# Kernel optimization log

Measured on AMD Instinct MI355X. Metric: run time of the kernel, lower is better.

The kernel has to match this reference:

```python
import math
import jax, jax.numpy as jnp
import numpy as np

EMBED = 1024
HEAD = 1024  # embedding_dim // num_heads with num_heads=1


def setup_inputs() -> dict:
    key = jax.random.key(0)
    kx, kq, kk, kv = jax.random.split(key, 4)
    x = jax.random.normal(kx, (8, 2048, EMBED), dtype=jnp.float32)
    padding_mask = jnp.ones((8, 2048), dtype=jnp.float32)
    Q = 0.02 * jax.random.normal(kq, (EMBED, HEAD), dtype=jnp.float32)
    K = 0.02 * jax.random.normal(kk, (EMBED, HEAD), dtype=jnp.float32)
    V = 0.02 * jax.random.normal(kv, (EMBED, HEAD), dtype=jnp.float32)
    return {"x": x, "padding_mask": padding_mask, "Q": Q, "K": K, "V": V}


def reference(x, padding_mask, Q, K, V):
    # x: [B, S, E]; Q/K/V: [E, H]; padding_mask: [B, S]
    q = x @ Q  # [B, S, H]
    k = x @ K
    v = x @ V
    scores = jnp.einsum("bsh,bth->bst", q, k)  # [B, S, S]
    # faithful to torch: mask = tril(scores) * padding_mask.unsqueeze(1)
    mask = jnp.tril(scores) * padding_mask[:, None, :]
    scores = jnp.where(mask == 0, -1e9, scores)
    weights = jax.nn.softmax(scores / math.sqrt(k.shape[-1]), axis=-1)
    return weights @ v  # [B, S, H]
```

## Files before the change

kernel.cpp:

```cpp
#include <hip/hip_runtime.h>
#include <hip/hip_bf16.h>


using bf16 = __hip_bfloat16;
typedef __attribute__((ext_vector_type(8))) short short8;
typedef __attribute__((ext_vector_type(4))) unsigned short ushort4_t;
typedef __attribute__((ext_vector_type(4))) float f32x4;

#define BATCH 8
#define SEQ   2048
#define EMB   1024
#define HEADD 1024

__device__ __forceinline__ unsigned short f2bf(float x) {
  bf16 h = __float2bfloat16(x);
  return *reinterpret_cast<unsigned short*>(&h);
}
__device__ __forceinline__ float bf2f(unsigned short u) {
  unsigned int v = ((unsigned int)u) << 16;
  return *reinterpret_cast<float*>(&v);
}

__device__ __forceinline__ void gload_lds16(const bf16* g, bf16* l) {
  __builtin_amdgcn_global_load_lds(
      (const __attribute__((address_space(1))) void*)g,
      (__attribute__((address_space(3))) void*)l, 16, 0, 0);
}

__device__ __forceinline__ int xcd_swz(int wg, int nwg) {
  int q = nwg >> 3, r = nwg & 7;
  int x = wg & 7, o = wg >> 3;
  return (x < r ? x * (q + 1) : r * (q + 1) + (x - r) * q) + o;
}

__global__ __launch_bounds__(256) void cast_x(const float* __restrict__ in,
                                              bf16* __restrict__ out, int n4) {
  for (int i = blockIdx.x * 256 + threadIdx.x; i < n4; i += gridDim.x * 256) {
    float4 v = ((const float4*)in)[i];
    ushort4_t o;
    o[0] = f2bf(v.x); o[1] = f2bf(v.y); o[2] = f2bf(v.z); o[3] = f2bf(v.w);
    *(ushort4_t*)(out + 4 * (long)i) = o;
  }
}

__global__ __launch_bounds__(256) void transpose_w(const float* __restrict__ Qw,
                                                   const float* __restrict__ Kw,
                                                   const float* __restrict__ Vw,
                                                   bf16* __restrict__ wbT) {
  const float* W = blockIdx.z == 0 ? Qw : (blockIdx.z == 1 ? Kw : Vw);
  __shared__ float t[32][33];
  int e0 = blockIdx.x * 32, h0 = blockIdx.y * 32;
  int c = threadIdx.x & 31, r8 = threadIdx.x >> 5;
#pragma unroll
  for (int i = 0; i < 4; ++i) {
    int r = r8 + i * 8;
    t[r][c] = W[(long)(e0 + r) * HEADD + h0 + c];
  }
  __syncthreads();
#pragma unroll
  for (int i = 0; i < 4; ++i) {
    int r = r8 + i * 8;
    wbT[((long)blockIdx.z * HEADD + h0 + r) * EMB + e0 + c] = __float2bfloat16(t[c][r]);
  }
}


__device__ __forceinline__ void rd4(const char* base, const unsigned* offs, short8* dst) {
#pragma unroll
  for (int i = 0; i < 4; ++i) dst[i] = *(const short8*)(base + offs[i]);
}

#define BARR __builtin_amdgcn_s_barrier()
#define LGKM0 asm volatile("s_waitcnt lgkmcnt(0)")
#define VMW(n) asm volatile("s_waitcnt vmcnt(" #n ")")

__global__ __launch_bounds__(512, 2) void gemm_qkv(
    const bf16* __restrict__ A, long lda,
    const bf16* __restrict__ Bm, long ldb,
    bf16* __restrict__ Cp, long ldc, int K,
    int nbj, bf16* __restrict__ vTp) {
  const int wg = xcd_swz(blockIdx.x, gridDim.x);
  const int bi = wg / nbj, bj = wg % nbj;
  const int i0 = bi * 256, j0 = bj * 256;
  const int tid = threadIdx.x;
  const int wave = tid >> 6, lane = tid & 63;
  const int wr2 = wave >> 2, wc4 = wave & 3;
  const int lrow = lane & 15, li16 = lane >> 4;

  const bf16* Ab = A + (long)i0 * lda;
  const bf16* Bb = Bm + (long)j0 * ldb;

  __shared__ bf16 sm[2][2][2][8192];
  const char* smr = (const char*)&sm[0][0][0][0];
  char* smw = (char*)&sm[0][0][0][0];

  unsigned aoff[2][4], boff[4];
#pragma unroll
  for (int ch = 0; ch < 2; ++ch)
#pragma unroll
    for (int m = 0; m < 4; ++m) {
      int row = ch * 128 + wr2 * 64 + m * 16 + lrow, mr = row >> 1;
      int s = (((row & 1) << 2) | li16) ^ (mr & 7);
      aoff[ch][m] = (unsigned)(mr * 128 + s * 16);
    }
#pragma unroll
  for (int n = 0; n < 4; ++n) {
    int row = wc4 * 64 + n * 16 + lrow, mr = row >> 1;
    int s = (((row & 1) << 2) | li16) ^ (mr & 7);
    boff[n] = (unsigned)(32768 + mr * 128 + s * 16);
  }

  const int mr0 = tid >> 3, og0 = (tid & 7) ^ (mr0 & 7);
  const int r0 = mr0 * 2 + (og0 >> 2), cb0 = (og0 & 3) * 8;
  const int mr1 = 64 + (tid >> 3), og1 = (tid & 7) ^ (mr1 & 7);
  const int r1 = mr1 * 2 + (og1 >> 2), cb1 = (og1 & 3) * 8;
  const bf16* gA0 = Ab + (long)r0 * lda + cb0;
  const bf16* gA1 = Ab + (long)r1 * lda + cb1;
  const bf16* gB0 = Bb + (long)r0 * ldb + cb0;
  const bf16* gB1 = Bb + (long)r1 * ldb + cb1;
  const unsigned sd = (unsigned)tid * 16;

#define ST_ATOP(kx, bb) { gload_lds16(gA0 + (kx), (bf16*)(smw + (bb) + sd)); \
                          gload_lds16(gA0 + (kx) + 32, (bf16*)(smw + (bb) + 16384 + sd)); }
#define ST_ABOT(kx, bb) { gload_lds16(gA1 + (kx), (bf16*)(smw + (bb) + 8192 + sd)); \
                          gload_lds16(gA1 + (kx) + 32, (bf16*)(smw + (bb) + 16384 + 8192 + sd)); }
#define ST_BK(kx, kh, bb) { gload_lds16(gB0 + (kx) + (kh) * 32, (bf16*)(smw + (bb) + 32768 + (kh) * 16384 + sd)); \
                            gload_lds16(gB1 + (kx) + (kh) * 32, (bf16*)(smw + (bb) + 32768 + (kh) * 16384 + 8192 + sd)); }

  f32x4 acc[8][4];
#pragma unroll
  for (int mi = 0; mi < 8; ++mi)
#pragma unroll
    for (int ni = 0; ni < 4; ++ni) acc[mi][ni] = (f32x4){0.f, 0.f, 0.f, 0.f};

  const int np = (K / 64) >> 1;
  short8 a[4], b[4];

  ST_ATOP(0, 0); ST_ABOT(0, 0); ST_BK(0, 0, 0); ST_BK(0, 1, 0);
  ST_BK(64, 0, 65536); ST_ATOP(64, 65536);
  asm volatile("s_waitcnt vmcnt(4)" ::: "memory");
  asm volatile("s_barrier" ::: "memory");

  for (int t2 = 0; t2 < np; ++t2) {
    const bool tail = (t2 == np - 1);
    const long kT1 = (long)t2 * 128 + 64;
    const long kT2 = kT1 + 64, kT3 = kT1 + 128;

    rd4(smr, boff, b); rd4(smr, aoff[0], a);
    ST_ABOT(kT1, 65536); ST_BK(kT1, 1, 65536);
    BARR; LGKM0;
    __builtin_amdgcn_s_setprio(1);
#pragma unroll
    for (int m = 0; m < 4; ++m)
#pragma unroll
      for (int n = 0; n < 4; ++n)
        acc[m][n] = __builtin_amdgcn_mfma_f32_16x16x32_bf16(a[m], b[n], acc[m][n], 0, 0, 0);
    __builtin_amdgcn_s_setprio(0);
    BARR;
    rd4(smr, aoff[1], a);
    BARR; LGKM0;
    __builtin_amdgcn_s_setprio(1);
#pragma unroll
    for (int m = 0; m < 4; ++m)
#pragma unroll
      for (int n = 0; n < 4; ++n)
        acc[m + 4][n] = __builtin_amdgcn_mfma_f32_16x16x32_bf16(a[m], b[n], acc[m + 4][n], 0, 0, 0);
    __builtin_amdgcn_s_setprio(0);
    BARR;
    rd4(smr + 16384, boff, b); rd4(smr + 16384, aoff[0], a);
    if (!tail) ST_BK(kT2, 0, 0);
    BARR; LGKM0;
    __builtin_amdgcn_s_setprio(1);
#pragma unroll
    for (int m = 0; m < 4; ++m)
#pragma unroll
      for (int n = 0; n < 4; ++n)
        acc[m][n] = __builtin_amdgcn_mfma_f32_16x16x32_bf16(a[m], b[n], acc[m][n], 0, 0, 0);
    __builtin_amdgcn_s_setprio(0);
    BARR;
    rd4(smr + 16384, aoff[1], a);
    if (!tail) ST_ATOP(kT2, 0);
    BARR; LGKM0;
    __builtin_amdgcn_s_setprio(1);
#pragma unroll
    for (int m = 0; m < 4; ++m)
#pragma unroll
      for (int n = 0; n < 4; ++n)
        acc[m + 4][n] = __builtin_amdgcn_mfma_f32_16x16x32_bf16(a[m], b[n], acc[m + 4][n], 0, 0, 0);
    __builtin_amdgcn_s_setprio(0);
    if (tail) { VMW(0); } else { VMW(4); }
    BARR;
    rd4(smr + 65536, boff, b); rd4(smr + 65536, aoff[0], a);
    if (!tail) { ST_ABOT(kT2, 0); ST_BK(kT2, 1, 0); }
    BARR; LGKM0;
    __builtin_amdgcn_s_setprio(1);
#pragma unroll
    for (int m = 0; m < 4; ++m)
#pragma unroll
      for (int n = 0; n < 4; ++n)
        acc[m][n] = __builtin_amdgcn_mfma_f32_16x16x32_bf16(a[m], b[n], acc[m][n], 0, 0, 0);
    __builtin_amdgcn_s_setprio(0);
    BARR;
    rd4(smr + 65536, aoff[1], a);
    BARR; LGKM0;
    __builtin_amdgcn_s_setprio(1);
#pragma unroll
    for (int m = 0; m < 4; ++m)
#pragma unroll
      for (int n = 0; n < 4; ++n)
        acc[m + 4][n] = __builtin_amdgcn_mfma_f32_16x16x32_bf16(a[m], b[n], acc[m + 4][n], 0, 0, 0);
    __builtin_amdgcn_s_setprio(0);
    BARR;
    rd4(smr + 65536 + 16384, boff, b); rd4(smr + 65536 + 16384, aoff[0], a);
    if (!tail) ST_BK(kT3, 0, 65536);
    BARR; LGKM0;
    __builtin_amdgcn_s_setprio(1);
#pragma unroll
    for (int m = 0; m < 4; ++m)
#pragma unroll
      for (int n = 0; n < 4; ++n)
        acc[m][n] = __builtin_amdgcn_mfma_f32_16x16x32_bf16(a[m], b[n], acc[m][n], 0, 0, 0);
    __builtin_amdgcn_s_setprio(0);
    BARR;
    rd4(smr + 65536 + 16384, aoff[1], a);
    if (!tail) ST_ATOP(kT3, 65536);
    BARR; LGKM0;
    __builtin_amdgcn_s_setprio(1);
#pragma unroll
    for (int m = 0; m < 4; ++m)
#pragma unroll
      for (int n = 0; n < 4; ++n)
        acc[m + 4][n] = __builtin_amdgcn_mfma_f32_16x16x32_bf16(a[m], b[n], acc[m + 4][n], 0, 0, 0);
    __builtin_amdgcn_s_setprio(0);
    if (tail) { VMW(0); } else { VMW(4); }
    BARR;
  }

#pragma unroll
  for (int mi = 0; mi < 8; ++mi) {
    const int ch = mi >> 2, m = mi & 3;
    const int rowb = i0 + ch * 128 + wr2 * 64 + m * 16 + li16 * 4;
#pragma unroll
    for (int ni = 0; ni < 4; ++ni) {
      const int col = j0 + wc4 * 64 + ni * 16 + lrow;
      if (col < 2048) {
#pragma unroll
        for (int r = 0; r < 4; ++r)
          Cp[(long)(rowb + r) * ldc + col] = __float2bfloat16(acc[mi][ni][r]);
      } else {
        const int h = col - 2048;
        const int b2 = rowb >> 11, sr = rowb & 2047;
        ushort4_t o;
#pragma unroll
        for (int r = 0; r < 4; ++r) o[r] = f2bf(acc[mi][ni][r]);
        *(ushort4_t*)(vTp + ((long)b2 * HEADD + h) * SEQ + sr) = o;
      }
    }
  }
#undef ST_ATOP
#undef ST_ABOT
#undef ST_BK
}


template <int MODE, bool CAUSAL2, bool PAIRED_PV>
__global__ __launch_bounds__(256, 2) void gemm4w(
    const bf16* __restrict__ A, long aBatch, long lda,
    const bf16* __restrict__ Bm, long bBatch, long ldb,
    void* __restrict__ Cp, long cBatch, long ldc, int K,
    int tpb, const float* __restrict__ invr, float* __restrict__ psum) {
  int bz, bi, bj, ktn;
  if (PAIRED_PV) {
    const int g = blockIdx.x;
    const int s = g & 255, half = g >> 8;
    const int p = s >> 6, c = s & 63;
    bi = half ? (7 - p) : p;
    bj = c >> 3; bz = c & 7;
    ktn = 8 * (bi + 1);
  } else {
    const int wg = xcd_swz(blockIdx.x, gridDim.x);
    bz = wg / tpb;
    const int f = wg % tpb;
    if (CAUSAL2) {
      int i = 0, cum = 0;
      while (cum + 2 * i + 2 <= f) { cum += 2 * i + 2; ++i; }
      bi = i; bj = f - cum;
    } else {
      bi = f; bj = 0;
    }
    ktn = K / 32;
  }
  const int i0 = bi * 256, j0 = bj * 128;
  const int tid = threadIdx.x;
  const int wave = tid >> 6, lane = tid & 63;
  const int wr = wave >> 1, wc = wave & 1;
  const int lrow = lane & 15, li16 = lane >> 4;

  const bf16* Ab = A + (long)bz * aBatch + (long)i0 * lda;
  const bf16* Bb = Bm + (long)bz * bBatch + (long)j0 * ldb;

  __shared__ char smc[65536];
  const char* smr = smc;
  char* smw = smc;

  unsigned aoff[8], boff[4];
#pragma unroll
  for (int m = 0; m < 8; ++m) {
    int row = wr * 128 + m * 16 + lrow, mr = row >> 1;
    int s = (((row & 1) << 2) | li16) ^ (mr & 7);
    aoff[m] = (unsigned)(mr * 128 + s * 16);
  }
#pragma unroll
  for (int n = 0; n < 4; ++n) {
    int row = wc * 64 + n * 16 + lrow, mr = row >> 1;
    int s = (((row & 1) << 2) | li16) ^ (mr & 7);
    boff[n] = (unsigned)(16384 + mr * 128 + s * 16);
  }

  const bf16* gA[4];
  const bf16* gB[2];
#pragma unroll
  for (int l = 0; l < 4; ++l) {
    int mr = l * 32 + (tid >> 3), og = (tid & 7) ^ (mr & 7);
    gA[l] = Ab + (long)(mr * 2 + (og >> 2)) * lda + (og & 3) * 8;
  }
#pragma unroll
  for (int l = 0; l < 2; ++l) {
    int mr = l * 32 + (tid >> 3), og = (tid & 7) ^ (mr & 7);
    gB[l] = Bb + (long)(mr * 2 + (og >> 2)) * ldb + (og & 3) * 8;
  }
  const unsigned sda = (unsigned)tid * 16;

  f32x4 acc[8][4];
#pragma unroll
  for (int mi = 0; mi < 8; ++mi)
#pragma unroll
    for (int ni = 0; ni < 4; ++ni) acc[mi][ni] = (f32x4){0.f, 0.f, 0.f, 0.f};

#pragma unroll
  for (int l = 0; l < 4; ++l) gload_lds16(gA[l], (bf16*)(smw + l * 4096 + sda));
#pragma unroll
  for (int l = 0; l < 2; ++l) gload_lds16(gB[l], (bf16*)(smw + 16384 + l * 4096 + sda));
  asm volatile("s_waitcnt vmcnt(0)" ::: "memory");
  asm volatile("s_barrier" ::: "memory");

  unsigned nxto = 32768;
  short8 a[8], b[4];

  for (int t = 0; t < ktn; ++t) {
    const bool pre = (t + 1 < ktn);
    const int kn = (t + 1) * 32;

#pragma unroll
    for (int n = 0; n < 4; ++n) b[n] = *(const short8*)(smr + boff[n]);
#pragma unroll
    for (int m = 0; m < 8; ++m) a[m] = *(const short8*)(smr + aoff[m]);
    if (pre) {
#pragma unroll
      for (int l = 0; l < 4; ++l)
        gload_lds16(gA[l] + kn, (bf16*)(smw + nxto + l * 4096 + sda));
#pragma unroll
      for (int l = 0; l < 2; ++l)
        gload_lds16(gB[l] + kn, (bf16*)(smw + nxto + 16384 + l * 4096 + sda));
    }
    __builtin_amdgcn_s_setprio(1);
#pragma unroll
    for (int m = 0; m < 8; ++m)
#pragma unroll
      for (int n = 0; n < 4; ++n)
        acc[m][n] = __builtin_amdgcn_mfma_f32_16x16x32_bf16(a[m], b[n], acc[m][n], 0, 0, 0);
    __builtin_amdgcn_s_setprio(0);
    if (pre) {
      asm volatile("s_waitcnt vmcnt(0)");
      __builtin_amdgcn_s_barrier();
#pragma unroll
      for (int m = 0; m < 8; ++m) aoff[m] ^= 32768u;
#pragma unroll
      for (int n = 0; n < 4; ++n) boff[n] ^= 32768u;
      nxto ^= 32768u;
    }
  }

  if constexpr (MODE == 0) {
#pragma unroll
    for (int mi = 0; mi < 8; ++mi) {
      const int rowb = i0 + wr * 128 + mi * 16 + li16 * 4;
      float* C = (float*)Cp + (long)bz * cBatch;
      const float4 iv = *(const float4*)(invr + bz * SEQ + rowb);
#pragma unroll
      for (int ni = 0; ni < 4; ++ni) {
        const int col = j0 + wc * 64 + ni * 16 + lrow;
        C[(long)(rowb + 0) * ldc + col] = acc[mi][ni][0] * iv.x;
        C[(long)(rowb + 1) * ldc + col] = acc[mi][ni][1] * iv.y;
        C[(long)(rowb + 2) * ldc + col] = acc[mi][ni][2] * iv.z;
        C[(long)(rowb + 3) * ldc + col] = acc[mi][ni][3] * iv.w;
      }
    }
  } else {
    bf16* C = (bf16*)Cp + (long)bz * cBatch;
    const float sc = 0.03125f;
#pragma unroll
    for (int mi = 0; mi < 8; ++mi) {
      const int rowb = i0 + wr * 128 + mi * 16 + li16 * 4;
      float rs0 = 0.f, rs1 = 0.f, rs2 = 0.f, rs3 = 0.f;
#pragma unroll
      for (int ni = 0; ni < 4; ++ni) {
        const int col = j0 + wc * 64 + ni * 16 + lrow;
#pragma unroll
        for (int r = 0; r < 4; ++r) {
          const int row = rowb + r;
          float p = (col <= row) ? __expf(acc[mi][ni][r] * sc) : 0.f;
          if (r == 0) rs0 += p; else if (r == 1) rs1 += p;
          else if (r == 2) rs2 += p; else rs3 += p;
          C[(long)row * ldc + col] = __float2bfloat16(p);
        }
      }
#pragma unroll
      for (int o = 1; o < 16; o <<= 1) {
        rs0 += __shfl_xor(rs0, o);
        rs1 += __shfl_xor(rs1, o);
        rs2 += __shfl_xor(rs2, o);
        rs3 += __shfl_xor(rs3, o);
      }
      if (lrow == 0) {
        const int slot = (j0 >> 6) + wc;
        float* ps = psum + ((long)bz * SEQ + rowb) * 32 + slot;
        ps[0 * 32] = rs0;
        ps[1 * 32] = rs1;
        ps[2 * 32] = rs2;
        ps[3 * 32] = rs3;
      }
    }
  }
}

__global__ __launch_bounds__(256) void invr_k(const float* __restrict__ psum,
                                              float* __restrict__ invr) {
  const int idx = blockIdx.x * 256 + threadIdx.x;
  const int s = idx & 2047;
  const int nv = (s >> 6) + 1;
  const float* p = psum + (long)idx * 32;
  float sum = 0.f;
  for (int v = 0; v < nv; ++v) sum += p[v];
  invr[idx] = 1.f / sum;
}

extern "C" void kernel_launch(void* const* d_in, const int* in_sizes, int n_in,
                              void* d_out, int out_size, void* d_ws, size_t ws_size,
                              hipStream_t stream) {
  const float* x = (const float*)d_in[0];
  const float* Qw = (const float*)d_in[2];
  const float* Kw = (const float*)d_in[3];
  const float* Vw = (const float*)d_in[4];
  float* out = (float*)d_out;

  char* ws = (char*)d_ws;
  bf16* xb  = (bf16*)(ws + 0);
  float* ivr = (float*)(ws + 0);
  float* psm = (float*)(ws + 65536);
  bf16* wbT = (bf16*)(ws + 33554432);
  bf16* qk  = (bf16*)(ws + 39845888);
  bf16* vT  = (bf16*)(ws + 106954752);
  bf16* P   = (bf16*)(ws + 140509184);

  cast_x<<<2048, 256, 0, stream>>>(x, xb, (BATCH * SEQ * EMB) / 4);
  transpose_w<<<dim3(32, 32, 3), 256, 0, stream>>>(Qw, Kw, Vw, wbT);

  gemm_qkv<<<768, 512, 0, stream>>>(xb, EMB, wbT, EMB, qk, 2048, EMB, 12, vT);

  gemm4w<1, true, false><<<576, 256, 0, stream>>>(
      qk, (long)SEQ * 2048, 2048, qk + 1024, (long)SEQ * 2048, 2048,
      P, (long)SEQ * SEQ, SEQ, EMB, 72, nullptr, psm);

  invr_k<<<64, 256, 0, stream>>>(psm, ivr);

  gemm4w<0, false, true><<<512, 256, 0, stream>>>(
      P, (long)SEQ * SEQ, SEQ, vT, (long)HEADD * SEQ, SEQ,
      out, (long)SEQ * HEADD, HEADD, SEQ, 0, ivr, nullptr);
}
```

Measured before the change: 254.7 us.

## Fold Q·Kᵀ into a precomputed weight so scores use x directly

Precomputes W = Q·Kᵀ (as a split-K GEMM over 1024x1024 weights followed by a reduction kernel), then projects x only once through W and V instead of through Q, K and V. Scores are formed as (xW)·xᵀ against the bf16 x buffer, so the projection GEMM shrinks from three 1024-wide outputs to two. This removes a third of the projection GEMM work, at the cost of an extra small GEMM, a reduction pass, and an extra bf16 rounding of the combined weight, which may change numerics.

```diff
diff --git a/kernel.cpp b/kernel.cpp
--- a/kernel.cpp
+++ b/kernel.cpp
@@ -43,25 +43,37 @@
   }
 }
 
-__global__ __launch_bounds__(256) void transpose_w(const float* __restrict__ Qw,
-                                                   const float* __restrict__ Kw,
-                                                   const float* __restrict__ Vw,
-                                                   bf16* __restrict__ wbT) {
-  const float* W = blockIdx.z == 0 ? Qw : (blockIdx.z == 1 ? Kw : Vw);
+__global__ __launch_bounds__(256) void transpose_v(const float* __restrict__ src,
+                                                   bf16* __restrict__ dst) {
   __shared__ float t[32][33];
   int e0 = blockIdx.x * 32, h0 = blockIdx.y * 32;
   int c = threadIdx.x & 31, r8 = threadIdx.x >> 5;
 #pragma unroll
   for (int i = 0; i < 4; ++i) {
     int r = r8 + i * 8;
-    t[r][c] = W[(long)(e0 + r) * HEADD + h0 + c];
+    t[r][c] = src[(long)(e0 + r) * HEADD + h0 + c];
   }
   __syncthreads();
 #pragma unroll
   for (int i = 0; i < 4; ++i) {
     int r = r8 + i * 8;
-    wbT[((long)blockIdx.z * HEADD + h0 + r) * EMB + e0 + c] = __float2bfloat16(t[c][r]);
-  }
+    dst[(long)(h0 + r) * EMB + e0 + c] = __float2bfloat16(t[c][r]);
+  }
+}
+
+__global__ __launch_bounds__(256) void wqk_reduce(const float* __restrict__ part,
+                                                  bf16* __restrict__ out) {
+  const int i = blockIdx.x * 256 + threadIdx.x;
+  const float4* p = (const float4*)part;
+  float4 s = p[i];
+#pragma unroll
+  for (int ks = 1; ks < 8; ++ks) {
+    float4 v = p[(long)ks * 262144 + i];
+    s.x += v.x; s.y += v.y; s.z += v.z; s.w += v.w;
+  }
+  ushort4_t o;
+  o[0] = f2bf(s.x); o[1] = f2bf(s.y); o[2] = f2bf(s.z); o[3] = f2bf(s.w);
+  *(ushort4_t*)(out + 4 * (long)i) = o;
 }
 
 
@@ -243,12 +255,12 @@
 #pragma unroll
     for (int ni = 0; ni < 4; ++ni) {
       const int col = j0 + wc4 * 64 + ni * 16 + lrow;
-      if (col < 2048) {
+      if (col < 1024) {
 #pragma unroll
         for (int r = 0; r < 4; ++r)
           Cp[(long)(rowb + r) * ldc + col] = __float2bfloat16(acc[mi][ni][r]);
       } else {
-        const int h = col - 2048;
+        const int h = col - 1024;
         const int b2 = rowb >> 11, sr = rowb & 2047;
         ushort4_t o;
 #pragma unroll
@@ -263,14 +275,21 @@
 }
 
 
-template <int MODE, bool CAUSAL2, bool PAIRED_PV>
+template <int MODE, bool CAUSAL2, bool PAIRED_PV, bool WSPLIT>
 __global__ __launch_bounds__(256, 2) void gemm4w(
     const bf16* __restrict__ A, long aBatch, long lda,
     const bf16* __restrict__ Bm, long bBatch, long ldb,
     void* __restrict__ Cp, long cBatch, long ldc, int K,
     int tpb, const float* __restrict__ invr, float* __restrict__ psum) {
-  int bz, bi, bj, ktn;
-  if (PAIRED_PV) {
+  int bz, bi, bj, ktn, koff = 0;
+  if (WSPLIT) {
+    const int g = blockIdx.x;
+    bz = g >> 5;
+    const int r = g & 31;
+    bi = r >> 3; bj = r & 7;
+    ktn = 4;
+    koff = bz * 128;
+  } else if (PAIRED_PV) {
     const int g = blockIdx.x;
     const int s = g & 255, half = g >> 8;
     const int p = s >> 6, c = s & 63;
@@ -296,8 +315,8 @@
   const int wr = wave >> 1, wc = wave & 1;
   const int lrow = lane & 15, li16 = lane >> 4;
 
-  const bf16* Ab = A + (long)bz * aBatch + (long)i0 * lda;
-  const bf16* Bb = Bm + (long)bz * bBatch + (long)j0 * ldb;
+  const bf16* Ab = A + (WSPLIT ? 0L : (long)bz * aBatch) + (long)i0 * lda + koff;
+  const bf16* Bb = Bm + (WSPLIT ? 0L : (long)bz * bBatch) + (long)j0 * ldb + koff;
 
   __shared__ char smc[65536];
   const char* smr = smc;
@@ -394,6 +413,19 @@
         C[(long)(rowb + 1) * ldc + col] = acc[mi][ni][1] * iv.y;
         C[(long)(rowb + 2) * ldc + col] = acc[mi][ni][2] * iv.z;
         C[(long)(rowb + 3) * ldc + col] = acc[mi][ni][3] * iv.w;
+      }
+    }
+  } else if constexpr (MODE == 2) {
+    float* C = (float*)Cp + (long)bz * cBatch;
+#pragma unroll
+    for (int mi = 0; mi < 8; ++mi) {
+      const int rowb = i0 + wr * 128 + mi * 16 + li16 * 4;
+#pragma unroll
+      for (int ni = 0; ni < 4; ++ni) {
+        const int col = j0 + wc * 64 + ni * 16 + lrow;
+#pragma unroll
+        for (int r = 0; r < 4; ++r)
+          C[(long)(rowb + r) * ldc + col] = acc[mi][ni][r];
       }
     }
   } else {
@@ -455,26 +487,36 @@
   float* out = (float*)d_out;
 
   char* ws = (char*)d_ws;
-  bf16* xb  = (bf16*)(ws + 0);
-  float* ivr = (float*)(ws + 0);
-  float* psm = (float*)(ws + 65536);
-  bf16* wbT = (bf16*)(ws + 33554432);
-  bf16* qk  = (bf16*)(ws + 39845888);
-  bf16* vT  = (bf16*)(ws + 106954752);
-  bf16* P   = (bf16*)(ws + 140509184);
+  bf16*  xb  = (bf16*)(ws + 0);
+  bf16*  qp  = (bf16*)(ws + 33554432);
+  bf16*  vT  = (bf16*)(ws + 67108864);
+  bf16*  P   = (bf16*)(ws + 100663296);
+  float* Wp  = (float*)(ws + 100663296);
+  bf16*  Wb  = (bf16*)(ws + 167772160);
+  bf16*  qb  = (bf16*)(ws + 171966464);
+  bf16*  kb  = (bf16*)(ws + 174063616);
+  float* psm = (float*)(ws + 176160768);
+  float* ivr = (float*)(ws + 178257920);
 
   cast_x<<<2048, 256, 0, stream>>>(x, xb, (BATCH * SEQ * EMB) / 4);
-  transpose_w<<<dim3(32, 32, 3), 256, 0, stream>>>(Qw, Kw, Vw, wbT);
-
-  gemm_qkv<<<768, 512, 0, stream>>>(xb, EMB, wbT, EMB, qk, 2048, EMB, 12, vT);
-
-  gemm4w<1, true, false><<<576, 256, 0, stream>>>(
-      qk, (long)SEQ * 2048, 2048, qk + 1024, (long)SEQ * 2048, 2048,
+  cast_x<<<1024, 256, 0, stream>>>(Qw, qb, (EMB * HEADD) / 4);
+  cast_x<<<1024, 256, 0, stream>>>(Kw, kb, (EMB * HEADD) / 4);
+  transpose_v<<<dim3(32, 32), 256, 0, stream>>>(Vw, Wb + (long)1024 * EMB);
+
+  gemm4w<2, false, false, true><<<256, 256, 0, stream>>>(
+      kb, 0L, HEADD, qb, 0L, HEADD, Wp, (long)1024 * 1024, 1024, 1024,
+      0, nullptr, nullptr);
+  wqk_reduce<<<1024, 256, 0, stream>>>(Wp, Wb);
+
+  gemm_qkv<<<512, 512, 0, stream>>>(xb, EMB, Wb, EMB, qp, 1024, EMB, 8, vT);
+
+  gemm4w<1, true, false, false><<<576, 256, 0, stream>>>(
+      qp, (long)SEQ * 1024, 1024, xb, (long)SEQ * 1024, 1024,
       P, (long)SEQ * SEQ, SEQ, EMB, 72, nullptr, psm);
 
   invr_k<<<64, 256, 0, stream>>>(psm, ivr);
 
-  gemm4w<0, false, true><<<512, 256, 0, stream>>>(
+  gemm4w<0, false, true, false><<<512, 256, 0, stream>>>(
       P, (long)SEQ * SEQ, SEQ, vT, (long)HEADD * SEQ, SEQ,
       out, (long)SEQ * HEADD, HEADD, SEQ, 0, ivr, nullptr);
 }
```

After: 241.2 us. 5.3% less time.
